# Optimization experiments

Hardware: AMD Instinct MI355X
Metric: run time of the kernel (lower is better)

## Reference

```python
import jax, jax.numpy as jnp
import numpy as np

JITTER = 1e-05
TOL = 1e-04
MAX_ITER = 10
TAYLOR_ORDER = 5


def _safe_eigh(A):
    # torch safe_eigh: first attempt always adds jitter*I (eigh on SPD never fails, so first try succeeds)
    D = A.shape[-1]
    return jnp.linalg.eigh(A + JITTER * jnp.eye(D, dtype=A.dtype))


def _rebuild(vecs, vals):
    # vecs @ diag(vals) @ vecs^T, batched
    return jnp.einsum('...ij,...j,...kj->...ik', vecs, vals, vecs)


def matrix_sqrt(A):
    vals, vecs = _safe_eigh(A)
    return _rebuild(vecs, jnp.sqrt(jnp.clip(vals, JITTER)))


def matrix_inv_sqrt(A):
    vals, vecs = _safe_eigh(A)
    return _rebuild(vecs, 1.0 / jnp.sqrt(jnp.clip(vals, JITTER)))


def enforce_spd(M):
    vals, vecs = _safe_eigh(M)
    M2 = _rebuild(vecs, jnp.clip(vals, JITTER))
    return (M2 + jnp.swapaxes(M2, -1, -2)) * 0.5


def expm_taylor(Xm):
    D = Xm.shape[-1]
    I = jnp.broadcast_to(jnp.eye(D, dtype=Xm.dtype), Xm.shape)
    out = I
    Xp = I
    fac = 1.0
    for i in range(1, TAYLOR_ORDER + 1):
        Xp = Xp @ Xm
        fac *= i
        out = out + Xp / fac
    return out


def karcher_mean(X):
    # X: (B, N, D, D) SPD matrices -> (B, D, D) Riemannian (Karcher) mean
    B, N, D, _ = X.shape
    G0 = X.mean(axis=1)

    def step(carry, _):
        G, done = carry
        G_sqrt = matrix_sqrt(G)
        G_is = matrix_inv_sqrt(G)
        # A[b,n] = G_is[b] @ X[b,n] @ G_is[b]
        A = jnp.einsum('bij,bnjk,bkl->bnil', G_is, X, G_is)
        vals, vecs = _safe_eigh(A)
        logA = _rebuild(vecs, jnp.log(jnp.clip(vals, JITTER)))  # (B,N,D,D)
        Delta = logA.mean(axis=1)  # (B,D,D)
        norm_Delta = jnp.sqrt(jnp.sum(Delta * Delta, axis=(-2, -1))).mean()
        G_new = enforce_spd(G_sqrt @ expm_taylor(Delta) @ G_sqrt)
        # torch updates G, THEN checks break -> freeze only once done was set in a previous iter
        G_next = jnp.where(done, G, G_new)
        done_next = jnp.logical_or(done, norm_Delta < TOL)
        return (G_next, done_next), None

    (G, _), _ = jax.lax.scan(step, (G0, jnp.array(False)), None, length=MAX_ITER)
    return G


def setup_inputs() -> dict:
    key = jax.random.key(0)
    B, N, D = 64, 512, 32
    A = jax.random.normal(key, (B, N, D, D), dtype=jnp.float32)
    # well-conditioned SPD inputs, as an SPD pooling layer would receive
    X = A @ jnp.swapaxes(A, -1, -2) / D + 0.5 * jnp.eye(D, dtype=jnp.float32)
    return {"X": X}


def reference(X) -> jnp.ndarray:
    return karcher_mean(X)
```

## Files before the change

kernel.cpp:

```cpp
#include <hip/hip_runtime.h>
#include <math.h>

#define BB 64
#define NN 512
#define DD 32
#define LD2 36
#define LDG 32
#define JIT 1e-5f
#define TOLF 1e-4f
#define MAXIT 10
#define DSPLIT 10

__device__ __forceinline__ float bpf(int addr, float v) {
    return __int_as_float(__builtin_amdgcn_ds_bpermute(addr, __float_as_int(v)));
}

__device__ __forceinline__ float swz16(float x) {
    return __int_as_float(__builtin_amdgcn_ds_swizzle(__float_as_int(x), 0x401F));
}

__device__ __forceinline__ float xhsum(float x) {
    unsigned u = __float_as_uint(x);
    auto r = __builtin_amdgcn_permlane32_swap(u, u, false, false);
    return __uint_as_float(r[0]) + __uint_as_float(r[1]);
}

__device__ __forceinline__ float xhmax(float x) {
    unsigned u = __float_as_uint(x);
    auto r = __builtin_amdgcn_permlane32_swap(u, u, false, false);
    return fmaxf(__uint_as_float(r[0]), __uint_as_float(r[1]));
}

__device__ __forceinline__ void wsync() {
    __asm__ volatile("s_waitcnt lgkmcnt(0)" ::: "memory");
}

template<int CTRL>
__device__ __forceinline__ float dppf(float x) {
    int i = __float_as_int(x);
    return __int_as_float(__builtin_amdgcn_update_dpp(i, i, CTRL, 0xF, 0xF, true));
}

__device__ __forceinline__ float part16(float x, bool hi16) {
#if __has_builtin(__builtin_amdgcn_permlane16_swap)
    unsigned u = __float_as_uint(x);
    auto r = __builtin_amdgcn_permlane16_swap(u, u, false, false);
    return hi16 ? __uint_as_float(r[0]) : __uint_as_float(r[1]);
#else
    return swz16(x);
#endif
}

__device__ __forceinline__ float max16pair(float x) {
#if __has_builtin(__builtin_amdgcn_permlane16_swap)
    unsigned u = __float_as_uint(x);
    auto r = __builtin_amdgcn_permlane16_swap(u, u, false, false);
    return fmaxf(__uint_as_float(r[0]), __uint_as_float(r[1]));
#else
    return fmaxf(x, swz16(x));
#endif
}

template<int LOW>
__device__ __forceinline__ float xorlane_lo(float x) {
    float v = x;
    if constexpr (LOW == 1)  v = dppf<0xB1>(v);
    else if constexpr (LOW == 2)  v = dppf<0x4E>(v);
    else if constexpr (LOW == 3)  v = dppf<0x1B>(v);
    else if constexpr (LOW == 4)  { v = dppf<0x141>(v); v = dppf<0x1B>(v); }
    else if constexpr (LOW == 5)  { v = dppf<0x141>(v); v = dppf<0x4E>(v); }
    else if constexpr (LOW == 6)  { v = dppf<0x141>(v); v = dppf<0xB1>(v); }
    else if constexpr (LOW == 7)  v = dppf<0x141>(v);
    else if constexpr (LOW == 8)  v = dppf<0x128>(v);
    else if constexpr (LOW == 9)  { v = dppf<0x128>(v); v = dppf<0xB1>(v); }
    else if constexpr (LOW == 10) { v = dppf<0x128>(v); v = dppf<0x4E>(v); }
    else if constexpr (LOW == 11) { v = dppf<0x128>(v); v = dppf<0x1B>(v); }
    else if constexpr (LOW == 12) { v = dppf<0x140>(v); v = dppf<0x1B>(v); }
    else if constexpr (LOW == 13) { v = dppf<0x140>(v); v = dppf<0x4E>(v); }
    else if constexpr (LOW == 14) { v = dppf<0x140>(v); v = dppf<0xB1>(v); }
    else if constexpr (LOW == 15) v = dppf<0x140>(v);
    return v;
}

__device__ __forceinline__ float redmax32(float x) {
    x = fmaxf(x, dppf<0xB1>(x));
    x = fmaxf(x, dppf<0x4E>(x));
    x = fmaxf(x, dppf<0x124>(x));
    x = fmaxf(x, dppf<0x128>(x));
    x = max16pair(x);
    return xhmax(x);
}

template<int M>
__device__ __forceinline__ void rot_step(float a[16], int c, bool hi16, float& maxrel) {
    constexpr int LOW = M & 15;
    float pa[16];
    if constexpr (M < 16) {
#pragma unroll
        for (int i = 0; i < 16; ++i) pa[i] = xorlane_lo<M>(a[i]);
    } else {
#pragma unroll
        for (int i = 0; i < 16; ++i) {
            float t = xorlane_lo<LOW>(a[i]);
            pa[i] = (i < DSPLIT) ? swz16(t) : part16(t, hi16);
        }
    }
    float gs = 0.f, gc = 0.f;
#pragma unroll
    for (int i = 0; i < 16; ++i) {
        gs = fmaf(a[i], a[i], gs);
        gc = fmaf(a[i], pa[i], gc);
    }
    gs = xhsum(gs);
    gc = xhsum(gc);
    float gp;
    if constexpr (M < 16) gp = xorlane_lo<M>(gs);
    else                  gp = swz16(xorlane_lo<LOW>(gs));
    bool isP = c < (c ^ M);
    float gpp = isP ? gs : gp;
    float gqq = isP ? gp : gs;
    float rel = gc * gc * __builtin_amdgcn_rcpf(gpp * gqq);
    maxrel = fmaxf(maxrel, rel);
    float tau = (gqq - gpp) * (0.5f * __builtin_amdgcn_rcpf(gc));
    float den = fabsf(tau) + __builtin_amdgcn_sqrtf(fmaf(tau, tau, 1.f));
    float tt  = copysignf(__builtin_amdgcn_rcpf(den), tau);
    tt = (rel > 1e-24f) ? tt : 0.f;
    float cs  = __builtin_amdgcn_rsqf(fmaf(tt, tt, 1.f));
    float sn  = tt * cs;
    float sg = isP ? -sn : sn;
#pragma unroll
    for (int i = 0; i < 16; ++i) a[i] = fmaf(sg, pa[i], cs * a[i]);
}

__device__ __forceinline__ void jac1(float a[16], int c, bool hi16,
                                     int maxsweep, float thr) {
#pragma unroll 1
    for (int sweep = 0; sweep < maxsweep; ++sweep) {
        float maxrel = 0.f;
        rot_step<1>(a, c, hi16, maxrel);  rot_step<2>(a, c, hi16, maxrel);
        rot_step<3>(a, c, hi16, maxrel);  rot_step<4>(a, c, hi16, maxrel);
        rot_step<5>(a, c, hi16, maxrel);  rot_step<6>(a, c, hi16, maxrel);
        rot_step<7>(a, c, hi16, maxrel);  rot_step<8>(a, c, hi16, maxrel);
        rot_step<9>(a, c, hi16, maxrel);  rot_step<10>(a, c, hi16, maxrel);
        rot_step<11>(a, c, hi16, maxrel); rot_step<12>(a, c, hi16, maxrel);
        rot_step<13>(a, c, hi16, maxrel); rot_step<14>(a, c, hi16, maxrel);
        rot_step<15>(a, c, hi16, maxrel); rot_step<16>(a, c, hi16, maxrel);
        rot_step<17>(a, c, hi16, maxrel); rot_step<18>(a, c, hi16, maxrel);
        rot_step<19>(a, c, hi16, maxrel); rot_step<20>(a, c, hi16, maxrel);
        rot_step<21>(a, c, hi16, maxrel); rot_step<22>(a, c, hi16, maxrel);
        rot_step<23>(a, c, hi16, maxrel); rot_step<24>(a, c, hi16, maxrel);
        rot_step<25>(a, c, hi16, maxrel); rot_step<26>(a, c, hi16, maxrel);
        rot_step<27>(a, c, hi16, maxrel); rot_step<28>(a, c, hi16, maxrel);
        rot_step<29>(a, c, hi16, maxrel); rot_step<30>(a, c, hi16, maxrel);
        rot_step<31>(a, c, hi16, maxrel);
        maxrel = redmax32(maxrel);
        if (maxrel < thr) break;
    }
}

__device__ __forceinline__ void mm32w(const float* A, const float* B, float* C, int lane) {
    int r = lane >> 1, cb = (lane & 1) << 4;
    float acc[16];
#pragma unroll
    for (int j = 0; j < 16; ++j) acc[j] = 0.0f;
    for (int k = 0; k < DD; ++k) {
        float a = A[r * LD2 + k];
        const float4* Br = (const float4*)(B + k * LD2 + cb);
        float4 b0 = Br[0], b1 = Br[1], b2 = Br[2], b3 = Br[3];
        acc[0]  = fmaf(a, b0.x, acc[0]);  acc[1]  = fmaf(a, b0.y, acc[1]);
        acc[2]  = fmaf(a, b0.z, acc[2]);  acc[3]  = fmaf(a, b0.w, acc[3]);
        acc[4]  = fmaf(a, b1.x, acc[4]);  acc[5]  = fmaf(a, b1.y, acc[5]);
        acc[6]  = fmaf(a, b1.z, acc[6]);  acc[7]  = fmaf(a, b1.w, acc[7]);
        acc[8]  = fmaf(a, b2.x, acc[8]);  acc[9]  = fmaf(a, b2.y, acc[9]);
        acc[10] = fmaf(a, b2.z, acc[10]); acc[11] = fmaf(a, b2.w, acc[11]);
        acc[12] = fmaf(a, b3.x, acc[12]); acc[13] = fmaf(a, b3.y, acc[13]);
        acc[14] = fmaf(a, b3.z, acc[14]); acc[15] = fmaf(a, b3.w, acc[15]);
    }
    wsync();
    float4* Cr = (float4*)(C + r * LD2 + cb);
    Cr[0] = make_float4(acc[0],  acc[1],  acc[2],  acc[3]);
    Cr[1] = make_float4(acc[4],  acc[5],  acc[6],  acc[7]);
    Cr[2] = make_float4(acc[8],  acc[9],  acc[10], acc[11]);
    Cr[3] = make_float4(acc[12], acc[13], acc[14], acc[15]);
    wsync();
}


__global__ __launch_bounds__(256) void k0_zero(float* __restrict__ G, int* __restrict__ done,
                                               float* __restrict__ norm_acc, int* __restrict__ cnt_all,
                                               int* __restrict__ cnt_b) {
    float4* Gb = (float4*)(G + blockIdx.x * 1024);
    Gb[threadIdx.x] = make_float4(0.f, 0.f, 0.f, 0.f);
    if (blockIdx.x == 0) {
        if (threadIdx.x == 0) { *done = 0; *norm_acc = 0.f; *cnt_all = 0; }
        if (threadIdx.x < BB) cnt_b[threadIdx.x] = 0;
    }
}

__global__ __launch_bounds__(256) void k0_mean(const float* __restrict__ X, float* __restrict__ G) {
    int blk = blockIdx.x;
    int b = blk >> 3, chunk = blk & 7;
    int t = threadIdx.x;
    const float4* Xb = (const float4*)(X + ((size_t)(b * NN + chunk * 64)) * 1024);
    float4 acc = make_float4(0.f, 0.f, 0.f, 0.f);
    for (int n = 0; n < 64; ++n) {
        float4 v = Xb[n * 256 + t];
        acc.x += v.x; acc.y += v.y; acc.z += v.z; acc.w += v.w;
    }
    const float inv = 1.0f / NN;
    float* Gb = G + b * 1024 + t * 4;
    atomicAdd(Gb + 0, acc.x * inv);
    atomicAdd(Gb + 1, acc.y * inv);
    atomicAdd(Gb + 2, acc.z * inv);
    atomicAdd(Gb + 3, acc.w * inv);
}


__global__ __launch_bounds__(64) void k1_init(const float* __restrict__ G,
                                              float* __restrict__ Gs, float* __restrict__ Gis,
                                              float* __restrict__ Vg) {
    int b = blockIdx.x, lane = threadIdx.x;
    int c = lane & 31, h = lane >> 5;
    bool hi16 = (lane & 16) != 0;
    int r = lane >> 1, cb = (lane & 1) << 4;
    __shared__ __align__(16) float sW[DD * LD2];
    __shared__ float sc1[DD], sc2[DD];

    float a[16];
    {
        const float4* Gc = (const float4*)(G + b * 1024 + c * 32 + 16 * h);
        float4 v0 = Gc[0], v1 = Gc[1], v2 = Gc[2], v3 = Gc[3];
        a[0]=v0.x; a[1]=v0.y; a[2]=v0.z; a[3]=v0.w;
        a[4]=v1.x; a[5]=v1.y; a[6]=v1.z; a[7]=v1.w;
        a[8]=v2.x; a[9]=v2.y; a[10]=v2.z; a[11]=v2.w;
        a[12]=v3.x; a[13]=v3.y; a[14]=v3.z; a[15]=v3.w;
#pragma unroll
        for (int i = 0; i < 16; ++i)
            if (16 * h + i == c) a[i] += JIT;
    }
    jac1(a, c, hi16, 10, 1e-12f);
    float gs2 = 0.f;
#pragma unroll
    for (int i = 0; i < 16; ++i) gs2 = fmaf(a[i], a[i], gs2);
    gs2 = xhsum(gs2);
    float l  = __builtin_amdgcn_sqrtf(gs2);
    float lc = fmaxf(l, JIT);
    float ig = __builtin_amdgcn_rcpf(gs2);
    float c1 = __builtin_amdgcn_sqrtf(lc) * ig;
    float c2 = __builtin_amdgcn_rsqf(lc) * ig;
    if (Vg) {
        float inl = __builtin_amdgcn_rsqf(gs2);
        float4* Vp = (float4*)(Vg + b * 1024 + c * 32 + 16 * h);
        Vp[0] = make_float4(a[0]*inl,  a[1]*inl,  a[2]*inl,  a[3]*inl);
        Vp[1] = make_float4(a[4]*inl,  a[5]*inl,  a[6]*inl,  a[7]*inl);
        Vp[2] = make_float4(a[8]*inl,  a[9]*inl,  a[10]*inl, a[11]*inl);
        Vp[3] = make_float4(a[12]*inl, a[13]*inl, a[14]*inl, a[15]*inl);
    }
    {
        float4* wp = (float4*)&sW[c * LD2 + 16 * h];
        wp[0] = make_float4(a[0],  a[1],  a[2],  a[3]);
        wp[1] = make_float4(a[4],  a[5],  a[6],  a[7]);
        wp[2] = make_float4(a[8],  a[9],  a[10], a[11]);
        wp[3] = make_float4(a[12], a[13], a[14], a[15]);
        if (h == 0) { sc1[c] = c1; sc2[c] = c2; }
    }
    wsync();
    float a1[16], a2[16];
#pragma unroll
    for (int j = 0; j < 16; ++j) { a1[j] = 0.f; a2[j] = 0.f; }
    for (int k = 0; k < DD; ++k) {
        float wr = sW[k * LD2 + r];
        float t1 = wr * sc1[k], t2 = wr * sc2[k];
        const float4* Wc = (const float4*)&sW[k * LD2 + cb];
        float4 w0 = Wc[0], w1 = Wc[1], w2 = Wc[2], w3 = Wc[3];
        a1[0]+=t1*w0.x; a2[0]+=t2*w0.x;  a1[1]+=t1*w0.y; a2[1]+=t2*w0.y;
        a1[2]+=t1*w0.z; a2[2]+=t2*w0.z;  a1[3]+=t1*w0.w; a2[3]+=t2*w0.w;
        a1[4]+=t1*w1.x; a2[4]+=t2*w1.x;  a1[5]+=t1*w1.y; a2[5]+=t2*w1.y;
        a1[6]+=t1*w1.z; a2[6]+=t2*w1.z;  a1[7]+=t1*w1.w; a2[7]+=t2*w1.w;
        a1[8]+=t1*w2.x; a2[8]+=t2*w2.x;  a1[9]+=t1*w2.y; a2[9]+=t2*w2.y;
        a1[10]+=t1*w2.z; a2[10]+=t2*w2.z; a1[11]+=t1*w2.w; a2[11]+=t2*w2.w;
        a1[12]+=t1*w3.x; a2[12]+=t2*w3.x; a1[13]+=t1*w3.y; a2[13]+=t2*w3.y;
        a1[14]+=t1*w3.z; a2[14]+=t2*w3.z; a1[15]+=t1*w3.w; a2[15]+=t2*w3.w;
    }
    float4* Gsb  = (float4*)(Gs  + b * 1024 + lane * 16);
    float4* Gisb = (float4*)(Gis + b * 1024 + lane * 16);
#pragma unroll
    for (int j4 = 0; j4 < 4; ++j4) {
        Gsb[j4]  = make_float4(a1[4*j4], a1[4*j4+1], a1[4*j4+2], a1[4*j4+3]);
        Gisb[j4] = make_float4(a2[4*j4], a2[4*j4+1], a2[4*j4+2], a2[4*j4+3]);
    }
}


__global__ __launch_bounds__(512, 4) void k2_log_acc(const float* __restrict__ X,
                                                     float* G, float* Gs, float* Gis,
                                                     float* __restrict__ Part,
                                                     int* __restrict__ done,
                                                     float* __restrict__ Vbuf,
                                                     float* __restrict__ Vg,
                                                     float* __restrict__ norm_acc,
                                                     int* __restrict__ cnt_all,
                                                     int* __restrict__ cnt_b,
                                                     int it) {
    if (*done) return;
    int b = blockIdx.x >> 4, grp = blockIdx.x & 15;
    int wv = threadIdx.x >> 6, lane = threadIdx.x & 63;
    int c = lane & 31, h = lane >> 5;
    bool hi16 = (lane & 16) != 0;
    int aself = lane << 2;

    __shared__ __align__(16) float sG[DD * LDG];
    __shared__ __align__(16) float sAall[8][DD * LD2];
    float* sA = sAall[wv];

    if (threadIdx.x < 256)
        ((float4*)sG)[threadIdx.x] = ((const float4*)(Gis + b * 1024))[threadIdx.x];
    __syncthreads();

    int r = lane >> 1, cb = (lane & 1) << 4;
    float dacc[16];
#pragma unroll
    for (int j = 0; j < 16; ++j) dacc[j] = 0.f;

#pragma unroll 1
    for (int nn = 0; nn < 4; ++nn) {
        int n = grp * 32 + wv * 4 + nn;
        {
            const float4* Xv = (const float4*)(X + ((size_t)(b * NN + n)) * 1024);
            float4 v0 = Xv[lane * 4 + 0], v1 = Xv[lane * 4 + 1];
            float4 v2 = Xv[lane * 4 + 2], v3 = Xv[lane * 4 + 3];
            wsync();
            int e = lane * 16;
            float* d0 = &sA[(e >> 5) * LD2 + (e & 31)];
            *((float4*)d0)        = v0;
            *((float4*)(d0 + 4))  = v1;
            *((float4*)(d0 + 8))  = v2;
            *((float4*)(d0 + 12)) = v3;
            wsync();
        }
        {
            float acc[16];
#pragma unroll
            for (int j = 0; j < 16; ++j) acc[j] = 0.f;
            for (int k = 0; k < DD; ++k) {
                float a = sG[k * LDG + r];
                const float4* Br = (const float4*)(sA + k * LD2 + cb);
                float4 b0 = Br[0], b1 = Br[1], b2 = Br[2], b3 = Br[3];
                acc[0]  = fmaf(a, b0.x, acc[0]);  acc[1]  = fmaf(a, b0.y, acc[1]);
                acc[2]  = fmaf(a, b0.z, acc[2]);  acc[3]  = fmaf(a, b0.w, acc[3]);
                acc[4]  = fmaf(a, b1.x, acc[4]);  acc[5]  = fmaf(a, b1.y, acc[5]);
                acc[6]  = fmaf(a, b1.z, acc[6]);  acc[7]  = fmaf(a, b1.w, acc[7]);
                acc[8]  = fmaf(a, b2.x, acc[8]);  acc[9]  = fmaf(a, b2.y, acc[9]);
                acc[10] = fmaf(a, b2.z, acc[10]); acc[11] = fmaf(a, b2.w, acc[11]);
                acc[12] = fmaf(a, b3.x, acc[12]); acc[13] = fmaf(a, b3.y, acc[13]);
                acc[14] = fmaf(a, b3.z, acc[14]); acc[15] = fmaf(a, b3.w, acc[15]);
            }
            wsync();
            float4* Cr = (float4*)(sA + r * LD2 + cb);
            Cr[0] = make_float4(acc[0],  acc[1],  acc[2],  acc[3]);
            Cr[1] = make_float4(acc[4],  acc[5],  acc[6],  acc[7]);
            Cr[2] = make_float4(acc[8],  acc[9],  acc[10], acc[11]);
            Cr[3] = make_float4(acc[12], acc[13], acc[14], acc[15]);
            wsync();
        }
        {
            float acc[16];
#pragma unroll
            for (int j = 0; j < 16; ++j) acc[j] = 0.f;
            for (int k = 0; k < DD; ++k) {
                float a = sA[r * LD2 + k];
                const float4* Br = (const float4*)(sG + k * LDG + cb);
                float4 b0 = Br[0], b1 = Br[1], b2 = Br[2], b3 = Br[3];
                acc[0]  = fmaf(a, b0.x, acc[0]);  acc[1]  = fmaf(a, b0.y, acc[1]);
                acc[2]  = fmaf(a, b0.z, acc[2]);  acc[3]  = fmaf(a, b0.w, acc[3]);
                acc[4]  = fmaf(a, b1.x, acc[4]);  acc[5]  = fmaf(a, b1.y, acc[5]);
                acc[6]  = fmaf(a, b1.z, acc[6]);  acc[7]  = fmaf(a, b1.w, acc[7]);
                acc[8]  = fmaf(a, b2.x, acc[8]);  acc[9]  = fmaf(a, b2.y, acc[9]);
                acc[10] = fmaf(a, b2.z, acc[10]); acc[11] = fmaf(a, b2.w, acc[11]);
                acc[12] = fmaf(a, b3.x, acc[12]); acc[13] = fmaf(a, b3.y, acc[13]);
                acc[14] = fmaf(a, b3.z, acc[14]); acc[15] = fmaf(a, b3.w, acc[15]);
            }
            wsync();
            float4* Cr = (float4*)(sA + r * LD2 + cb);
            Cr[0] = make_float4(acc[0],  acc[1],  acc[2],  acc[3]);
            Cr[1] = make_float4(acc[4],  acc[5],  acc[6],  acc[7]);
            Cr[2] = make_float4(acc[8],  acc[9],  acc[10], acc[11]);
            Cr[3] = make_float4(acc[12], acc[13], acc[14], acc[15]);
            wsync();
        }
        float a[16];
        if (it == 0) {
            const float4* cp = (const float4*)&sA[c * LD2 + 16 * h];
            float4 t0 = cp[0], t1 = cp[1], t2 = cp[2], t3 = cp[3];
            float tr[16] = { t0.x,t0.y,t0.z,t0.w, t1.x,t1.y,t1.z,t1.w,
                             t2.x,t2.y,t2.z,t2.w, t3.x,t3.y,t3.z,t3.w };
#pragma unroll
            for (int i = 0; i < 16; ++i) {
                int row = 16 * h + i;
                float v = 0.5f * (sA[row * LD2 + c] + tr[i]);
                if (row == c) v = tr[i] + JIT;
                a[i] = v;
            }
        } else {
            float v[32];
            {
                const float4* Vp = (const float4*)(Vbuf + ((size_t)(b * NN + n)) * 1024 + c * 32);
#pragma unroll
                for (int j4 = 0; j4 < 8; ++j4) {
                    float4 t = Vp[j4];
                    v[4*j4] = t.x; v[4*j4+1] = t.y; v[4*j4+2] = t.z; v[4*j4+3] = t.w;
                }
            }
#pragma unroll
            for (int i = 0; i < 16; ++i) {
                const float4* Ar = (const float4*)&sA[(16 * h + i) * LD2];
                float s = 0.f;
#pragma unroll
                for (int j4 = 0; j4 < 8; ++j4) {
                    float4 q = Ar[j4];
                    s = fmaf(q.x, v[4*j4],   s);
                    s = fmaf(q.y, v[4*j4+1], s);
                    s = fmaf(q.z, v[4*j4+2], s);
                    s = fmaf(q.w, v[4*j4+3], s);
                }
                a[i] = fmaf(JIT, v[16 * h + i], s);
            }
        }

        jac1(a, c, hi16, 8, 1e-8f);

        {
            float gs2 = 0.f;
#pragma unroll
            for (int i = 0; i < 16; ++i) gs2 = fmaf(a[i], a[i], gs2);
            gs2 = xhsum(gs2);
            float gs2c = fmaxf(gs2, JIT * JIT);
            float tk = 0.5f * logf(gs2c) * __builtin_amdgcn_rcpf(gs2);
            if (Vbuf) {
                float inl = __builtin_amdgcn_rsqf(gs2);
                float4* Vp = (float4*)(Vbuf + ((size_t)(b * NN + n)) * 1024 + c * 32 + 16 * h);
                Vp[0] = make_float4(a[0]*inl,  a[1]*inl,  a[2]*inl,  a[3]*inl);
                Vp[1] = make_float4(a[4]*inl,  a[5]*inl,  a[6]*inl,  a[7]*inl);
                Vp[2] = make_float4(a[8]*inl,  a[9]*inl,  a[10]*inl, a[11]*inl);
                Vp[3] = make_float4(a[12]*inl, a[13]*inl, a[14]*inl, a[15]*inl);
            }
            wsync();
            float4* wp = (float4*)&sA[c * LD2 + 16 * h];
            wp[0] = make_float4(a[0],  a[1],  a[2],  a[3]);
            wp[1] = make_float4(a[4],  a[5],  a[6],  a[7]);
            wp[2] = make_float4(a[8],  a[9],  a[10], a[11]);
            wp[3] = make_float4(a[12], a[13], a[14], a[15]);
            if (h == 0) sA[c * LD2 + 32] = tk;
            wsync();
            for (int k = 0; k < DD; ++k) {
                float t1 = sA[k * LD2 + r] * sA[k * LD2 + 32];
                const float4* Wr = (const float4*)&sA[k * LD2 + cb];
                float4 w0 = Wr[0], w1 = Wr[1], w2 = Wr[2], w3 = Wr[3];
                dacc[0]  = fmaf(t1, w0.x, dacc[0]);  dacc[1]  = fmaf(t1, w0.y, dacc[1]);
                dacc[2]  = fmaf(t1, w0.z, dacc[2]);  dacc[3]  = fmaf(t1, w0.w, dacc[3]);
                dacc[4]  = fmaf(t1, w1.x, dacc[4]);  dacc[5]  = fmaf(t1, w1.y, dacc[5]);
                dacc[6]  = fmaf(t1, w1.z, dacc[6]);  dacc[7]  = fmaf(t1, w1.w, dacc[7]);
                dacc[8]  = fmaf(t1, w2.x, dacc[8]);  dacc[9]  = fmaf(t1, w2.y, dacc[9]);
                dacc[10] = fmaf(t1, w2.z, dacc[10]); dacc[11] = fmaf(t1, w2.w, dacc[11]);
                dacc[12] = fmaf(t1, w3.x, dacc[12]); dacc[13] = fmaf(t1, w3.y, dacc[13]);
                dacc[14] = fmaf(t1, w3.z, dacc[14]); dacc[15] = fmaf(t1, w3.w, dacc[15]);
            }
        }
    }
    wsync();

    {
        float4* fp = (float4*)&sA[lane * 16];
        fp[0] = make_float4(dacc[0],  dacc[1],  dacc[2],  dacc[3]);
        fp[1] = make_float4(dacc[4],  dacc[5],  dacc[6],  dacc[7]);
        fp[2] = make_float4(dacc[8],  dacc[9],  dacc[10], dacc[11]);
        fp[3] = make_float4(dacc[12], dacc[13], dacc[14], dacc[15]);
    }
    __syncthreads();
    if (threadIdx.x < 256) {
        int t = threadIdx.x;
        float4 s0 = ((float4*)sAall[0])[t];
        float4 s1 = ((float4*)sAall[1])[t];
        float4 s2 = ((float4*)sAall[2])[t];
        float4 s3 = ((float4*)sAall[3])[t];
        float4 s4 = ((float4*)sAall[4])[t];
        float4 s5 = ((float4*)sAall[5])[t];
        float4 s6 = ((float4*)sAall[6])[t];
        float4 s7 = ((float4*)sAall[7])[t];
        float4 s;
        s.x = ((s0.x + s1.x) + (s2.x + s3.x)) + ((s4.x + s5.x) + (s6.x + s7.x));
        s.y = ((s0.y + s1.y) + (s2.y + s3.y)) + ((s4.y + s5.y) + (s6.y + s7.y));
        s.z = ((s0.z + s1.z) + (s2.z + s3.z)) + ((s4.z + s5.z) + (s6.z + s7.z));
        s.w = ((s0.w + s1.w) + (s2.w + s3.w)) + ((s4.w + s5.w) + (s6.w + s7.w));
        ((float4*)(Part + (size_t)blockIdx.x * 1024))[t] = s;
    }

    int* winp = (int*)sG;
    if (threadIdx.x == 0) *winp = 0;
    __syncthreads();
    if (threadIdx.x == 0) {
        __threadfence();
        int ret = atomicAdd(&cnt_b[b], 1);
        if (ret == 15) { *winp = 1; cnt_b[b] = 0; }
    }
    __syncthreads();
// ... 38 lines not shown
        }
        wsync();

        float outr[16];
#pragma unroll
        for (int j = 0; j < 16; ++j)
            outr[j] = ((cb + j) == r ? 1.0f : 0.0f) + d[j];
        float fac = 1.0f;
#pragma unroll 1
        for (int i = 2; i <= 5; ++i) {
            fac *= (float)i;
            float acc[16];
#pragma unroll
            for (int j = 0; j < 16; ++j) acc[j] = 0.f;
            const float* Xp = (i == 2) ? s0 : s1;
            for (int k = 0; k < DD; ++k) {
                float av = Xp[r * LD2 + k];
                const float4* Br = (const float4*)&s0[k * LD2 + cb];
                float4 b0 = Br[0], b1 = Br[1], b2 = Br[2], b3 = Br[3];
                acc[0]+=av*b0.x; acc[1]+=av*b0.y; acc[2]+=av*b0.z; acc[3]+=av*b0.w;
                acc[4]+=av*b1.x; acc[5]+=av*b1.y; acc[6]+=av*b1.z; acc[7]+=av*b1.w;
                acc[8]+=av*b2.x; acc[9]+=av*b2.y; acc[10]+=av*b2.z; acc[11]+=av*b2.w;
                acc[12]+=av*b3.x; acc[13]+=av*b3.y; acc[14]+=av*b3.z; acc[15]+=av*b3.w;
            }
            float invf = 1.0f / fac;
#pragma unroll
            for (int j = 0; j < 16; ++j) outr[j] = fmaf(acc[j], invf, outr[j]);
            wsync();
            float4* dp = (float4*)&s1[r * LD2 + cb];
            dp[0] = make_float4(acc[0],  acc[1],  acc[2],  acc[3]);
            dp[1] = make_float4(acc[4],  acc[5],  acc[6],  acc[7]);
            dp[2] = make_float4(acc[8],  acc[9],  acc[10], acc[11]);
            dp[3] = make_float4(acc[12], acc[13], acc[14], acc[15]);
            wsync();
        }
        {
            float4* dp = (float4*)&s0[r * LD2 + cb];
            dp[0] = make_float4(outr[0],  outr[1],  outr[2],  outr[3]);
            dp[1] = make_float4(outr[4],  outr[5],  outr[6],  outr[7]);
            dp[2] = make_float4(outr[8],  outr[9],  outr[10], outr[11]);
            dp[3] = make_float4(outr[12], outr[13], outr[14], outr[15]);
            const float4* Gsb = (const float4*)(Gs + b * 1024);
#pragma unroll
            for (int j4 = 0; j4 < 4; ++j4) {
                float4 v = Gsb[lane * 4 + j4];
                int e = lane * 16 + j4 * 4;
                *((float4*)&s1[(e >> 5) * LD2 + (e & 31)]) = v;
            }
        }
        wsync();
        mm32w(s1, s0, s2, lane);
        mm32w(s2, s1, s0, lane);

        float a[16];
        if (Vg == nullptr) {
#pragma unroll
            for (int i = 0; i < 16; ++i) {
                int row = 16 * h + i;
                float own = s0[c * LD2 + row];
                float v = 0.5f * (s0[row * LD2 + c] + own);
                if (row == c) v = own + JIT;
                a[i] = v;
            }
        } else {
            float v[32];
            {
                const float4* Vp = (const float4*)(Vg + b * 1024 + c * 32);
#pragma unroll
                for (int j4 = 0; j4 < 8; ++j4) {
                    float4 t = Vp[j4];
                    v[4*j4] = t.x; v[4*j4+1] = t.y; v[4*j4+2] = t.z; v[4*j4+3] = t.w;
                }
            }
#pragma unroll
            for (int i = 0; i < 16; ++i) {
                const float4* Mr = (const float4*)&s0[(16 * h + i) * LD2];
                float s = 0.f;
#pragma unroll
                for (int j4 = 0; j4 < 8; ++j4) {
                    float4 q = Mr[j4];
                    s = fmaf(q.x, v[4*j4],   s);
                    s = fmaf(q.y, v[4*j4+1], s);
                    s = fmaf(q.z, v[4*j4+2], s);
                    s = fmaf(q.w, v[4*j4+3], s);
                }
                a[i] = fmaf(JIT, v[16 * h + i], s);
            }
        }
        jac1(a, c, hi16, 10, 1e-12f);
        float gs2 = 0.f;
#pragma unroll
        for (int i = 0; i < 16; ++i) gs2 = fmaf(a[i], a[i], gs2);
        gs2 = xhsum(gs2);
        float l = __builtin_amdgcn_sqrtf(gs2);
        float clipl = fmaxf(l, JIT);
        float ig = __builtin_amdgcn_rcpf(gs2);
        float tg = clipl * ig;
        float sh = clipl + JIT;
        float ts = __builtin_amdgcn_sqrtf(sh) * ig;
        float ti = __builtin_amdgcn_rsqf(sh) * ig;
        if (Vg) {
            float inl = __builtin_amdgcn_rsqf(gs2);
            float4* Vp = (float4*)(Vg + b * 1024 + c * 32 + 16 * h);
            Vp[0] = make_float4(a[0]*inl,  a[1]*inl,  a[2]*inl,  a[3]*inl);
            Vp[1] = make_float4(a[4]*inl,  a[5]*inl,  a[6]*inl,  a[7]*inl);
            Vp[2] = make_float4(a[8]*inl,  a[9]*inl,  a[10]*inl, a[11]*inl);
            Vp[3] = make_float4(a[12]*inl, a[13]*inl, a[14]*inl, a[15]*inl);
        }
        wsync();
        {
            float4* wp = (float4*)&s1[c * LD2 + 16 * h];
            wp[0] = make_float4(a[0],  a[1],  a[2],  a[3]);
            wp[1] = make_float4(a[4],  a[5],  a[6],  a[7]);
            wp[2] = make_float4(a[8],  a[9],  a[10], a[11]);
            wp[3] = make_float4(a[12], a[13], a[14], a[15]);
            if (h == 0) { scof[c] = tg; scof[32 + c] = ts; scof[64 + c] = ti; }
        }
        wsync();
#pragma unroll 1
        for (int pass = 0; pass < 3; ++pass) {
            float g[16];
#pragma unroll
            for (int j = 0; j < 16; ++j) g[j] = 0.f;
            for (int k = 0; k < DD; ++k) {
                float t1 = s1[k * LD2 + r] * scof[pass * 32 + k];
                const float4* Wc = (const float4*)&s1[k * LD2 + cb];
                float4 w0 = Wc[0], w1 = Wc[1], w2 = Wc[2], w3 = Wc[3];
                g[0]+=t1*w0.x; g[1]+=t1*w0.y; g[2]+=t1*w0.z; g[3]+=t1*w0.w;
                g[4]+=t1*w1.x; g[5]+=t1*w1.y; g[6]+=t1*w1.z; g[7]+=t1*w1.w;
                g[8]+=t1*w2.x; g[9]+=t1*w2.y; g[10]+=t1*w2.z; g[11]+=t1*w2.w;
                g[12]+=t1*w3.x; g[13]+=t1*w3.y; g[14]+=t1*w3.z; g[15]+=t1*w3.w;
            }
            float* dst = (pass == 0) ? G : (pass == 1) ? Gs : Gis;
            float4* Db = (float4*)(dst + b * 1024 + lane * 16);
#pragma unroll
            for (int j4 = 0; j4 < 4; ++j4)
                Db[j4] = make_float4(g[4*j4], g[4*j4+1], g[4*j4+2], g[4*j4+3]);
        }

        __threadfence();
        if (lane == 0) {
            int r2 = atomicAdd(cnt_all, 1);
            if (r2 == BB - 1) {
                float nm = atomicAdd(norm_acc, 0.f);
                if (nm * (1.0f / BB) < TOLF) *done = 1;
                *norm_acc = 0.f;
                *cnt_all = 0;
                __threadfence();
            }
        }
    }
}

__global__ __launch_bounds__(256) void k5_out(const float* __restrict__ G, float* __restrict__ out) {
    int i = blockIdx.x * 256 + threadIdx.x;
    out[i] = G[i];
}

extern "C" void kernel_launch(void* const* d_in, const int* in_sizes, int n_in,
                              void* d_out, int out_size, void* d_ws, size_t ws_size,
                              hipStream_t stream) {
    const float* X = (const float*)d_in[0];
    float* ws = (float*)d_ws;
    float* G     = ws;
    float* Gs    = ws + 65536;
    float* Gis   = ws + 2 * 65536;
    float* Part  = ws + 3 * 65536;
    float* norm_acc = ws + 3 * 65536 + 1048576;
    int*   cnt_all  = (int*)(norm_acc + 1);
// ... 19 lines not shown
```

Baseline: 4.443 ms.

## Run two Jacobi eigensolves per wave with full 32-element columns per lane

Replaces the one-matrix-per-wave Jacobi solver, where each 32-element column was split across two half-waves, with a solver where each lane holds a full column. The two 32-lane halves of a wave each work on a different matrix at once. This drops the cross-half permlane reductions in every rotation and halves the number of sequential eigensolves in the main per-sample loop. The cost is twice the registers per lane (possible occupancy or spill pressure), a stage-in loop that builds each half's matrix in turn, and idle upper lanes in the single-matrix init and update kernels.

Result: no change. 4.455 ms (+0.3%).

```diff
diff --git a/kernel.cpp b/kernel.cpp
--- a/kernel.cpp
+++ b/kernel.cpp
@@ -9,7 +9,6 @@
 #define JIT 1e-5f
 #define TOLF 1e-4f
 #define MAXIT 10
-#define DSPLIT 10
 
 __device__ __forceinline__ float bpf(int addr, float v) {
     return __int_as_float(__builtin_amdgcn_ds_bpermute(addr, __float_as_int(v)));
@@ -92,29 +91,23 @@
 }
 
 template<int M>
-__device__ __forceinline__ void rot_step(float a[16], int c, bool hi16, float& maxrel) {
+__device__ __forceinline__ void rot32(float a[32], int c, bool hi16, float& maxrel) {
     constexpr int LOW = M & 15;
-    float pa[16];
-    if constexpr (M < 16) {
-#pragma unroll
-        for (int i = 0; i < 16; ++i) pa[i] = xorlane_lo<M>(a[i]);
-    } else {
-#pragma unroll
-        for (int i = 0; i < 16; ++i) {
-            float t = xorlane_lo<LOW>(a[i]);
-            pa[i] = (i < DSPLIT) ? swz16(t) : part16(t, hi16);
-        }
+    float pa[32];
+#pragma unroll
+    for (int i = 0; i < 32; ++i) {
+        float t = xorlane_lo<LOW>(a[i]);
+        if constexpr (M >= 16) pa[i] = (i < 16) ? swz16(t) : part16(t, hi16);
+        else                   pa[i] = t;
     }
     float gs = 0.f, gc = 0.f;
 #pragma unroll
-    for (int i = 0; i < 16; ++i) {
+    for (int i = 0; i < 32; ++i) {
         gs = fmaf(a[i], a[i], gs);
         gc = fmaf(a[i], pa[i], gc);
     }
-    gs = xhsum(gs);
-    gc = xhsum(gc);
     float gp;
-    if constexpr (M < 16) gp = xorlane_lo<M>(gs);
+    if constexpr (M < 16) gp = xorlane_lo<LOW>(gs);
     else                  gp = swz16(xorlane_lo<LOW>(gs));
     bool isP = c < (c ^ M);
     float gpp = isP ? gs : gp;
@@ -129,30 +122,30 @@
     float sn  = tt * cs;
     float sg = isP ? -sn : sn;
 #pragma unroll
-    for (int i = 0; i < 16; ++i) a[i] = fmaf(sg, pa[i], cs * a[i]);
-}
-
-__device__ __forceinline__ void jac1(float a[16], int c, bool hi16,
-                                     int maxsweep, float thr) {
+    for (int i = 0; i < 32; ++i) a[i] = fmaf(sg, pa[i], cs * a[i]);
+}
+
+__device__ __forceinline__ void jac_pair(float a[32], int c, bool hi16,
+                                         int maxsweep, float thr) {
 #pragma unroll 1
     for (int sweep = 0; sweep < maxsweep; ++sweep) {
         float maxrel = 0.f;
-        rot_step<1>(a, c, hi16, maxrel);  rot_step<2>(a, c, hi16, maxrel);
-        rot_step<3>(a, c, hi16, maxrel);  rot_step<4>(a, c, hi16, maxrel);
-        rot_step<5>(a, c, hi16, maxrel);  rot_step<6>(a, c, hi16, maxrel);
-        rot_step<7>(a, c, hi16, maxrel);  rot_step<8>(a, c, hi16, maxrel);
-        rot_step<9>(a, c, hi16, maxrel);  rot_step<10>(a, c, hi16, maxrel);
-        rot_step<11>(a, c, hi16, maxrel); rot_step<12>(a, c, hi16, maxrel);
-        rot_step<13>(a, c, hi16, maxrel); rot_step<14>(a, c, hi16, maxrel);
-        rot_step<15>(a, c, hi16, maxrel); rot_step<16>(a, c, hi16, maxrel);
-        rot_step<17>(a, c, hi16, maxrel); rot_step<18>(a, c, hi16, maxrel);
-        rot_step<19>(a, c, hi16, maxrel); rot_step<20>(a, c, hi16, maxrel);
-        rot_step<21>(a, c, hi16, maxrel); rot_step<22>(a, c, hi16, maxrel);
-        rot_step<23>(a, c, hi16, maxrel); rot_step<24>(a, c, hi16, maxrel);
-        rot_step<25>(a, c, hi16, maxrel); rot_step<26>(a, c, hi16, maxrel);
-        rot_step<27>(a, c, hi16, maxrel); rot_step<28>(a, c, hi16, maxrel);
-        rot_step<29>(a, c, hi16, maxrel); rot_step<30>(a, c, hi16, maxrel);
-        rot_step<31>(a, c, hi16, maxrel);
+        rot32<1>(a, c, hi16, maxrel);  rot32<2>(a, c, hi16, maxrel);
+        rot32<3>(a, c, hi16, maxrel);  rot32<4>(a, c, hi16, maxrel);
+        rot32<5>(a, c, hi16, maxrel);  rot32<6>(a, c, hi16, maxrel);
+        rot32<7>(a, c, hi16, maxrel);  rot32<8>(a, c, hi16, maxrel);
+        rot32<9>(a, c, hi16, maxrel);  rot32<10>(a, c, hi16, maxrel);
+        rot32<11>(a, c, hi16, maxrel); rot32<12>(a, c, hi16, maxrel);
+        rot32<13>(a, c, hi16, maxrel); rot32<14>(a, c, hi16, maxrel);
+        rot32<15>(a, c, hi16, maxrel); rot32<16>(a, c, hi16, maxrel);
+        rot32<17>(a, c, hi16, maxrel); rot32<18>(a, c, hi16, maxrel);
+        rot32<19>(a, c, hi16, maxrel); rot32<20>(a, c, hi16, maxrel);
+        rot32<21>(a, c, hi16, maxrel); rot32<22>(a, c, hi16, maxrel);
+        rot32<23>(a, c, hi16, maxrel); rot32<24>(a, c, hi16, maxrel);
+        rot32<25>(a, c, hi16, maxrel); rot32<26>(a, c, hi16, maxrel);
+        rot32<27>(a, c, hi16, maxrel); rot32<28>(a, c, hi16, maxrel);
+        rot32<29>(a, c, hi16, maxrel); rot32<30>(a, c, hi16, maxrel);
+        rot32<31>(a, c, hi16, maxrel);
         maxrel = redmax32(maxrel);
         if (maxrel < thr) break;
     }
@@ -220,49 +213,44 @@
                                               float* __restrict__ Gs, float* __restrict__ Gis,
                                               float* __restrict__ Vg) {
     int b = blockIdx.x, lane = threadIdx.x;
-    int c = lane & 31, h = lane >> 5;
+    int c = lane & 31;
     bool hi16 = (lane & 16) != 0;
     int r = lane >> 1, cb = (lane & 1) << 4;
     __shared__ __align__(16) float sW[DD * LD2];
     __shared__ float sc1[DD], sc2[DD];
 
-    float a[16];
+    float a[32];
     {
-        const float4* Gc = (const float4*)(G + b * 1024 + c * 32 + 16 * h);
-        float4 v0 = Gc[0], v1 = Gc[1], v2 = Gc[2], v3 = Gc[3];
-        a[0]=v0.x; a[1]=v0.y; a[2]=v0.z; a[3]=v0.w;
-        a[4]=v1.x; a[5]=v1.y; a[6]=v1.z; a[7]=v1.w;
-        a[8]=v2.x; a[9]=v2.y; a[10]=v2.z; a[11]=v2.w;
-        a[12]=v3.x; a[13]=v3.y; a[14]=v3.z; a[15]=v3.w;
-#pragma unroll
-        for (int i = 0; i < 16; ++i)
-            if (16 * h + i == c) a[i] += JIT;
-    }
-    jac1(a, c, hi16, 10, 1e-12f);
+        const float4* Gc = (const float4*)(G + b * 1024 + c * 32);
+#pragma unroll
+        for (int j4 = 0; j4 < 8; ++j4) {
+            float4 q = Gc[j4];
+            a[4*j4] = q.x; a[4*j4+1] = q.y; a[4*j4+2] = q.z; a[4*j4+3] = q.w;
+        }
+        a[c] += JIT;
+    }
+    jac_pair(a, c, hi16, 10, 1e-12f);
     float gs2 = 0.f;
 #pragma unroll
-    for (int i = 0; i < 16; ++i) gs2 = fmaf(a[i], a[i], gs2);
-    gs2 = xhsum(gs2);
+    for (int i = 0; i < 32; ++i) gs2 = fmaf(a[i], a[i], gs2);
     float l  = __builtin_amdgcn_sqrtf(gs2);
     float lc = fmaxf(l, JIT);
     float ig = __builtin_amdgcn_rcpf(gs2);
     float c1 = __builtin_amdgcn_sqrtf(lc) * ig;
     float c2 = __builtin_amdgcn_rsqf(lc) * ig;
-    if (Vg) {
+    if (Vg && lane < 32) {
         float inl = __builtin_amdgcn_rsqf(gs2);
-        float4* Vp = (float4*)(Vg + b * 1024 + c * 32 + 16 * h);
-        Vp[0] = make_float4(a[0]*inl,  a[1]*inl,  a[2]*inl,  a[3]*inl);
-        Vp[1] = make_float4(a[4]*inl,  a[5]*inl,  a[6]*inl,  a[7]*inl);
-        Vp[2] = make_float4(a[8]*inl,  a[9]*inl,  a[10]*inl, a[11]*inl);
-        Vp[3] = make_float4(a[12]*inl, a[13]*inl, a[14]*inl, a[15]*inl);
-    }
-    {
-        float4* wp = (float4*)&sW[c * LD2 + 16 * h];
-        wp[0] = make_float4(a[0],  a[1],  a[2],  a[3]);
-        wp[1] = make_float4(a[4],  a[5],  a[6],  a[7]);
-        wp[2] = make_float4(a[8],  a[9],  a[10], a[11]);
-        wp[3] = make_float4(a[12], a[13], a[14], a[15]);
-        if (h == 0) { sc1[c] = c1; sc2[c] = c2; }
+        float4* Vp = (float4*)(Vg + b * 1024 + c * 32);
+#pragma unroll
+        for (int j4 = 0; j4 < 8; ++j4)
+            Vp[j4] = make_float4(a[4*j4]*inl, a[4*j4+1]*inl, a[4*j4+2]*inl, a[4*j4+3]*inl);
+    }
+    if (lane < 32) {
+        float4* wp = (float4*)&sW[c * LD2];
+#pragma unroll
+        for (int j4 = 0; j4 < 8; ++j4)
+            wp[j4] = make_float4(a[4*j4], a[4*j4+1], a[4*j4+2], a[4*j4+3]);
+        sc1[c] = c1; sc2[c] = c2;
     }
     wsync();
     float a1[16], a2[16];
@@ -323,134 +311,140 @@
     for (int j = 0; j < 16; ++j) dacc[j] = 0.f;
 
 #pragma unroll 1
-    for (int nn = 0; nn < 4; ++nn) {
-        int n = grp * 32 + wv * 4 + nn;
-        {
-            const float4* Xv = (const float4*)(X + ((size_t)(b * NN + n)) * 1024);
-            float4 v0 = Xv[lane * 4 + 0], v1 = Xv[lane * 4 + 1];
-            float4 v2 = Xv[lane * 4 + 2], v3 = Xv[lane * 4 + 3];
+    for (int pp = 0; pp < 2; ++pp) {
+        int nb = grp * 32 + wv * 4 + pp * 2;
+        float a[32];
+#pragma unroll 1
+        for (int half = 0; half < 2; ++half) {
+            int n = nb + half;
+            {
+                const float4* Xv = (const float4*)(X + ((size_t)(b * NN + n)) * 1024);
+                float4 v0 = Xv[lane * 4 + 0], v1 = Xv[lane * 4 + 1];
+                float4 v2 = Xv[lane * 4 + 2], v3 = Xv[lane * 4 + 3];
+                wsync();
+                int e = lane * 16;
+                float* d0 = &sA[(e >> 5) * LD2 + (e & 31)];
+                *((float4*)d0)        = v0;
+                *((float4*)(d0 + 4))  = v1;
+                *((float4*)(d0 + 8))  = v2;
+                *((float4*)(d0 + 12)) = v3;
+                wsync();
+            }
+            {
+                float acc[16];
+#pragma unroll
+                for (int j = 0; j < 16; ++j) acc[j] = 0.f;
+                for (int k = 0; k < DD; ++k) {
+                    float av = sG[k * LDG + r];
+                    const float4* Br = (const float4*)(sA + k * LD2 + cb);
+                    float4 b0 = Br[0], b1 = Br[1], b2 = Br[2], b3 = Br[3];
+                    acc[0]  = fmaf(av, b0.x, acc[0]);  acc[1]  = fmaf(av, b0.y, acc[1]);
+                    acc[2]  = fmaf(av, b0.z, acc[2]);  acc[3]  = fmaf(av, b0.w, acc[3]);
+                    acc[4]  = fmaf(av, b1.x, acc[4]);  acc[5]  = fmaf(av, b1.y, acc[5]);
+                    acc[6]  = fmaf(av, b1.z, acc[6]);  acc[7]  = fmaf(av, b1.w, acc[7]);
+                    acc[8]  = fmaf(av, b2.x, acc[8]);  acc[9]  = fmaf(av, b2.y, acc[9]);
+                    acc[10] = fmaf(av, b2.z, acc[10]); acc[11] = fmaf(av, b2.w, acc[11]);
+                    acc[12] = fmaf(av, b3.x, acc[12]); acc[13] = fmaf(av, b3.y, acc[13]);
+                    acc[14] = fmaf(av, b3.z, acc[14]); acc[15] = fmaf(av, b3.w, acc[15]);
+                }
+                wsync();
+                float4* Cr = (float4*)(sA + r * LD2 + cb);
+                Cr[0] = make_float4(acc[0],  acc[1],  acc[2],  acc[3]);
+                Cr[1] = make_float4(acc[4],  acc[5],  acc[6],  acc[7]);
+                Cr[2] = make_float4(acc[8],  acc[9],  acc[10], acc[11]);
+                Cr[3] = make_float4(acc[12], acc[13], acc[14], acc[15]);
+                wsync();
+            }
+            {
+                float acc[16];
+#pragma unroll
+                for (int j = 0; j < 16; ++j) acc[j] = 0.f;
+                for (int k = 0; k < DD; ++k) {
+                    float av = sA[r * LD2 + k];
+                    const float4* Br = (const float4*)(sG + k * LDG + cb);
+                    float4 b0 = Br[0], b1 = Br[1], b2 = Br[2], b3 = Br[3];
+                    acc[0]  = fmaf(av, b0.x, acc[0]);  acc[1]  = fmaf(av, b0.y, acc[1]);
+                    acc[2]  = fmaf(av, b0.z, acc[2]);  acc[3]  = fmaf(av, b0.w, acc[3]);
+                    acc[4]  = fmaf(av, b1.x, acc[4]);  acc[5]  = fmaf(av, b1.y, acc[5]);
+                    acc[6]  = fmaf(av, b1.z, acc[6]);  acc[7]  = fmaf(av, b1.w, acc[7]);
+                    acc[8]  = fmaf(av, b2.x, acc[8]);  acc[9]  = fmaf(av, b2.y, acc[9]);
+                    acc[10] = fmaf(av, b2.z, acc[10]); acc[11] = fmaf(av, b2.w, acc[11]);
+                    acc[12] = fmaf(av, b3.x, acc[12]); acc[13] = fmaf(av, b3.y, acc[13]);
+                    acc[14] = fmaf(av, b3.z, acc[14]); acc[15] = fmaf(av, b3.w, acc[15]);
+                }
+                wsync();
+                float4* Cr = (float4*)(sA + r * LD2 + cb);
+                Cr[0] = make_float4(acc[0],  acc[1],  acc[2],  acc[3]);
+                Cr[1] = make_float4(acc[4],  acc[5],  acc[6],  acc[7]);
+                Cr[2] = make_float4(acc[8],  acc[9],  acc[10], acc[11]);
+                Cr[3] = make_float4(acc[12], acc[13], acc[14], acc[15]);
+                wsync();
+            }
+            if (h == half) {
+                if (it == 0) {
+                    float tr[32];
+                    const float4* rp = (const float4*)&sA[c * LD2];
+#pragma unroll
+                    for (int j4 = 0; j4 < 8; ++j4) {
+                        float4 q = rp[j4];
+                        tr[4*j4]=q.x; tr[4*j4+1]=q.y; tr[4*j4+2]=q.z; tr[4*j4+3]=q.w;
+                    }
+#pragma unroll
+                    for (int i = 0; i < 32; ++i) {
+                        float v = 0.5f * (sA[i * LD2 + c] + tr[i]);
+                        a[i] = (i == c) ? (tr[i] + JIT) : v;
+                    }
+                } else {
+                    float v[32];
+                    const float4* Vp = (const float4*)(Vbuf + ((size_t)(b * NN + n)) * 1024 + c * 32);
+#pragma unroll
+                    for (int j4 = 0; j4 < 8; ++j4) {
+                        float4 t = Vp[j4];
+                        v[4*j4]=t.x; v[4*j4+1]=t.y; v[4*j4+2]=t.z; v[4*j4+3]=t.w;
+                    }
+#pragma unroll
+                    for (int i = 0; i < 32; ++i) {
+                        const float4* Ar = (const float4*)&sA[i * LD2];
+                        float s = 0.f;
+#pragma unroll
+                        for (int j4 = 0; j4 < 8; ++j4) {
+                            float4 q = Ar[j4];
+                            s = fmaf(q.x, v[4*j4],   s);
+                            s = fmaf(q.y, v[4*j4+1], s);
+                            s = fmaf(q.z, v[4*j4+2], s);
+                            s = fmaf(q.w, v[4*j4+3], s);
+                        }
+                        a[i] = fmaf(JIT, v[i], s);
+                    }
+                }
+            }
+        }
+
+        jac_pair(a, c, hi16, 8, 1e-8f);
+
+        float gs2 = 0.f;
+#pragma unroll
+        for (int i = 0; i < 32; ++i) gs2 = fmaf(a[i], a[i], gs2);
+        float gs2c = fmaxf(gs2, JIT * JIT);
+        float tk = 0.5f * logf(gs2c) * __builtin_amdgcn_rcpf(gs2);
+        if (Vbuf) {
+            int n = nb + h;
+            float inl = __builtin_amdgcn_rsqf(gs2);
+            float4* Vp = (float4*)(Vbuf + ((size_t)(b * NN + n)) * 1024 + c * 32);
+#pragma unroll
+            for (int j4 = 0; j4 < 8; ++j4)
+                Vp[j4] = make_float4(a[4*j4]*inl, a[4*j4+1]*inl, a[4*j4+2]*inl, a[4*j4+3]*inl);
+        }
+#pragma unroll 1
+        for (int half = 0; half < 2; ++half) {
             wsync();
-            int e = lane * 16;
-            float* d0 = &sA[(e >> 5) * LD2 + (e & 31)];
-            *((float4*)d0)        = v0;
-            *((float4*)(d0 + 4))  = v1;
-            *((float4*)(d0 + 8))  = v2;
-            *((float4*)(d0 + 12)) = v3;
-            wsync();
-        }
-        {
-            float acc[16];
-#pragma unroll
-            for (int j = 0; j < 16; ++j) acc[j] = 0.f;
-            for (int k = 0; k < DD; ++k) {
-                float a = sG[k * LDG + r];
-                const float4* Br = (const float4*)(sA + k * LD2 + cb);
-                float4 b0 = Br[0], b1 = Br[1], b2 = Br[2], b3 = Br[3];
-                acc[0]  = fmaf(a, b0.x, acc[0]);  acc[1]  = fmaf(a, b0.y, acc[1]);
-                acc[2]  = fmaf(a, b0.z, acc[2]);  acc[3]  = fmaf(a, b0.w, acc[3]);
-                acc[4]  = fmaf(a, b1.x, acc[4]);  acc[5]  = fmaf(a, b1.y, acc[5]);
-                acc[6]  = fmaf(a, b1.z, acc[6]);  acc[7]  = fmaf(a, b1.w, acc[7]);
-                acc[8]  = fmaf(a, b2.x, acc[8]);  acc[9]  = fmaf(a, b2.y, acc[9]);
-                acc[10] = fmaf(a, b2.z, acc[10]); acc[11] = fmaf(a, b2.w, acc[11]);
-                acc[12] = fmaf(a, b3.x, acc[12]); acc[13] = fmaf(a, b3.y, acc[13]);
-                acc[14] = fmaf(a, b3.z, acc[14]); acc[15] = fmaf(a, b3.w, acc[15]);
-            }
-            wsync();
-            float4* Cr = (float4*)(sA + r * LD2 + cb);
-            Cr[0] = make_float4(acc[0],  acc[1],  acc[2],  acc[3]);
-            Cr[1] = make_float4(acc[4],  acc[5],  acc[6],  acc[7]);
-            Cr[2] = make_float4(acc[8],  acc[9],  acc[10], acc[11]);
-            Cr[3] = make_float4(acc[12], acc[13], acc[14], acc[15]);
-            wsync();
-        }
-        {
-            float acc[16];
-#pragma unroll
-            for (int j = 0; j < 16; ++j) acc[j] = 0.f;
-            for (int k = 0; k < DD; ++k) {
-                float a = sA[r * LD2 + k];
-                const float4* Br = (const float4*)(sG + k * LDG + cb);
-                float4 b0 = Br[0], b1 = Br[1], b2 = Br[2], b3 = Br[3];
-                acc[0]  = fmaf(a, b0.x, acc[0]);  acc[1]  = fmaf(a, b0.y, acc[1]);
-                acc[2]  = fmaf(a, b0.z, acc[2]);  acc[3]  = fmaf(a, b0.w, acc[3]);
-                acc[4]  = fmaf(a, b1.x, acc[4]);  acc[5]  = fmaf(a, b1.y, acc[5]);
-                acc[6]  = fmaf(a, b1.z, acc[6]);  acc[7]  = fmaf(a, b1.w, acc[7]);
-                acc[8]  = fmaf(a, b2.x, acc[8]);  acc[9]  = fmaf(a, b2.y, acc[9]);
-                acc[10] = fmaf(a, b2.z, acc[10]); acc[11] = fmaf(a, b2.w, acc[11]);
-                acc[12] = fmaf(a, b3.x, acc[12]); acc[13] = fmaf(a, b3.y, acc[13]);
-                acc[14] = fmaf(a, b3.z, acc[14]); acc[15] = fmaf(a, b3.w, acc[15]);
-            }
-            wsync();
-            float4* Cr = (float4*)(sA + r * LD2 + cb);
-            Cr[0] = make_float4(acc[0],  acc[1],  acc[2],  acc[3]);
-            Cr[1] = make_float4(acc[4],  acc[5],  acc[6],  acc[7]);
-            Cr[2] = make_float4(acc[8],  acc[9],  acc[10], acc[11]);
-            Cr[3] = make_float4(acc[12], acc[13], acc[14], acc[15]);
-            wsync();
-        }
-        float a[16];
-        if (it == 0) {
-            const float4* cp = (const float4*)&sA[c * LD2 + 16 * h];
-            float4 t0 = cp[0], t1 = cp[1], t2 = cp[2], t3 = cp[3];
-            float tr[16] = { t0.x,t0.y,t0.z,t0.w, t1.x,t1.y,t1.z,t1.w,
-                             t2.x,t2.y,t2.z,t2.w, t3.x,t3.y,t3.z,t3.w };
-#pragma unroll
-            for (int i = 0; i < 16; ++i) {
-                int row = 16 * h + i;
-                float v = 0.5f * (sA[row * LD2 + c] + tr[i]);
-                if (row == c) v = tr[i] + JIT;
-                a[i] = v;
-            }
-        } else {
-            float v[32];
-            {
-                const float4* Vp = (const float4*)(Vbuf + ((size_t)(b * NN + n)) * 1024 + c * 32);
-#pragma unroll
-                for (int j4 = 0; j4 < 8; ++j4) {
-                    float4 t = Vp[j4];
-                    v[4*j4] = t.x; v[4*j4+1] = t.y; v[4*j4+2] = t.z; v[4*j4+3] = t.w;
-                }
-            }
-#pragma unroll
-            for (int i = 0; i < 16; ++i) {
-                const float4* Ar = (const float4*)&sA[(16 * h + i) * LD2];
-                float s = 0.f;
-#pragma unroll
-                for (int j4 = 0; j4 < 8; ++j4) {
-                    float4 q = Ar[j4];
-                    s = fmaf(q.x, v[4*j4],   s);
-                    s = fmaf(q.y, v[4*j4+1], s);
-                    s = fmaf(q.z, v[4*j4+2], s);
-                    s = fmaf(q.w, v[4*j4+3], s);
-                }
-                a[i] = fmaf(JIT, v[16 * h + i], s);
-            }
-        }
-
-        jac1(a, c, hi16, 8, 1e-8f);
-
-        {
-            float gs2 = 0.f;
-#pragma unroll
-            for (int i = 0; i < 16; ++i) gs2 = fmaf(a[i], a[i], gs2);
-            gs2 = xhsum(gs2);
-            float gs2c = fmaxf(gs2, JIT * JIT);
-            float tk = 0.5f * logf(gs2c) * __builtin_amdgcn_rcpf(gs2);
-            if (Vbuf) {
-                float inl = __builtin_amdgcn_rsqf(gs2);
-                float4* Vp = (float4*)(Vbuf + ((size_t)(b * NN + n)) * 1024 + c * 32 + 16 * h);
-                Vp[0] = make_float4(a[0]*inl,  a[1]*inl,  a[2]*inl,  a[3]*inl);
-                Vp[1] = make_float4(a[4]*inl,  a[5]*inl,  a[6]*inl,  a[7]*inl);
-                Vp[2] = make_float4(a[8]*inl,  a[9]*inl,  a[10]*inl, a[11]*inl);
-                Vp[3] = make_float4(a[12]*inl, a[13]*inl, a[14]*inl, a[15]*inl);
-            }
-            wsync();
-            float4* wp = (float4*)&sA[c * LD2 + 16 * h];
-            wp[0] = make_float4(a[0],  a[1],  a[2],  a[3]);
-            wp[1] = make_float4(a[4],  a[5],  a[6],  a[7]);
-            wp[2] = make_float4(a[8],  a[9],  a[10], a[11]);
-            wp[3] = make_float4(a[12], a[13], a[14], a[15]);
-            if (h == 0) sA[c * LD2 + 32] = tk;
+            if (h == half) {
+                float4* wp = (float4*)&sA[c * LD2];
+#pragma unroll
+                for (int j4 = 0; j4 < 8; ++j4)
+                    wp[j4] = make_float4(a[4*j4], a[4*j4+1], a[4*j4+2], a[4*j4+3]);
+                sA[c * LD2 + 32] = tk;
+            }
             wsync();
             for (int k = 0; k < DD; ++k) {
                 float t1 = sA[k * LD2 + r] * sA[k * LD2 + 32];
@@ -595,29 +589,31 @@
         mm32w(s1, s0, s2, lane);
         mm32w(s2, s1, s0, lane);
 
-        float a[16];
+        float aa[32];
         if (Vg == nullptr) {
-#pragma unroll
-            for (int i = 0; i < 16; ++i) {
-                int row = 16 * h + i;
-                float own = s0[c * LD2 + row];
-                float v = 0.5f * (s0[row * LD2 + c] + own);
-                if (row == c) v = own + JIT;
-                a[i] = v;
+            float tr[32];
+            const float4* rp = (const float4*)&s0[c * LD2];
+#pragma unroll
+            for (int j4 = 0; j4 < 8; ++j4) {
+                float4 q = rp[j4];
+                tr[4*j4]=q.x; tr[4*j4+1]=q.y; tr[4*j4+2]=q.z; tr[4*j4+3]=q.w;
+            }
+#pragma unroll
+            for (int i = 0; i < 32; ++i) {
+                float v = 0.5f * (s0[i * LD2 + c] + tr[i]);
+                aa[i] = (i == c) ? (tr[i] + JIT) : v;
             }
         } else {
             float v[32];
-            {
-                const float4* Vp = (const float4*)(Vg + b * 1024 + c * 32);
-#pragma unroll
-                for (int j4 = 0; j4 < 8; ++j4) {
-                    float4 t = Vp[j4];
-                    v[4*j4] = t.x; v[4*j4+1] = t.y; v[4*j4+2] = t.z; v[4*j4+3] = t.w;
-                }
-            }
-#pragma unroll
-            for (int i = 0; i < 16; ++i) {
-                const float4* Mr = (const float4*)&s0[(16 * h + i) * LD2];
+            const float4* Vp = (const float4*)(Vg + b * 1024 + c * 32);
+#pragma unroll
+            for (int j4 = 0; j4 < 8; ++j4) {
+                float4 t = Vp[j4];
+                v[4*j4]=t.x; v[4*j4+1]=t.y; v[4*j4+2]=t.z; v[4*j4+3]=t.w;
+            }
+#pragma unroll
+            for (int i = 0; i < 32; ++i) {
+                const float4* Mr = (const float4*)&s0[i * LD2];
                 float s = 0.f;
 #pragma unroll
                 for (int j4 = 0; j4 < 8; ++j4) {
@@ -627,14 +623,13 @@
                     s = fmaf(q.z, v[4*j4+2], s);
                     s = fmaf(q.w, v[4*j4+3], s);
                 }
-                a[i] = fmaf(JIT, v[16 * h + i], s);
-            }
-        }
-        jac1(a, c, hi16, 10, 1e-12f);
+                aa[i] = fmaf(JIT, v[i], s);
+            }
+        }
+        jac_pair(aa, c, hi16, 10, 1e-12f);
         float gs2 = 0.f;
 #pragma unroll
-        for (int i = 0; i < 16; ++i) gs2 = fmaf(a[i], a[i], gs2);
-        gs2 = xhsum(gs2);
+        for (int i = 0; i < 32; ++i) gs2 = fmaf(aa[i], aa[i], gs2);
         float l = __builtin_amdgcn_sqrtf(gs2);
         float clipl = fmaxf(l, JIT);
         float ig = __builtin_amdgcn_rcpf(gs2);
@@ -642,22 +637,20 @@
         float sh = clipl + JIT;
         float ts = __builtin_amdgcn_sqrtf(sh) * ig;
         float ti = __builtin_amdgcn_rsqf(sh) * ig;
-        if (Vg) {
+        if (Vg && lane < 32) {
             float inl = __builtin_amdgcn_rsqf(gs2);
-            float4* Vp = (float4*)(Vg + b * 1024 + c * 32 + 16 * h);
-            Vp[0] = make_float4(a[0]*inl,  a[1]*inl,  a[2]*inl,  a[3]*inl);
-            Vp[1] = make_float4(a[4]*inl,  a[5]*inl,  a[6]*inl,  a[7]*inl);
-            Vp[2] = make_float4(a[8]*inl,  a[9]*inl,  a[10]*inl, a[11]*inl);
-            Vp[3] = make_float4(a[12]*inl, a[13]*inl, a[14]*inl, a[15]*inl);
+            float4* Vp = (float4*)(Vg + b * 1024 + c * 32);
+#pragma unroll
+            for (int j4 = 0; j4 < 8; ++j4)
+                Vp[j4] = make_float4(aa[4*j4]*inl, aa[4*j4+1]*inl, aa[4*j4+2]*inl, aa[4*j4+3]*inl);
         }
         wsync();
-        {
-            float4* wp = (float4*)&s1[c * LD2 + 16 * h];
-            wp[0] = make_float4(a[0],  a[1],  a[2],  a[3]);
-            wp[1] = make_float4(a[4],  a[5],  a[6],  a[7]);
-            wp[2] = make_float4(a[8],  a[9],  a[10], a[11]);
-            wp[3] = make_float4(a[12], a[13], a[14], a[15]);
-            if (h == 0) { scof[c] = tg; scof[32 + c] = ts; scof[64 + c] = ti; }
+        if (lane < 32) {
+            float4* wp = (float4*)&s1[c * LD2];
+#pragma unroll
+            for (int j4 = 0; j4 < 8; ++j4)
+                wp[j4] = make_float4(aa[4*j4], aa[4*j4+1], aa[4*j4+2], aa[4*j4+3]);
+            scof[c] = tg; scof[32 + c] = ts; scof[64 + c] = ti;
         }
         wsync();
 #pragma unroll 1
```
